# Performance work log

Measured on AMD Instinct MI355X. Metric: run time of the kernel, lower is better.

The kernel has to match this reference:

```python
import jax, jax.numpy as jnp
import numpy as np

N = 50000      # nodes
E = 1600000    # edges (avg degree 32)
DIN, DH, DOUT = 256, 128, 64


def gcn_conv(x, W, b, row, col, w, n):
    """One GCNConv layer (self-loops already appended to row/col/w).
    row = source nodes, col = target nodes; aggregate at targets."""
    xw = x @ W                                        # [n, d_out]
    deg = jax.ops.segment_sum(w, col, num_segments=n)  # in-degree weighted
    dinv = jnp.where(deg > 0, jax.lax.rsqrt(deg), 0.0)
    norm = dinv[row] * w * dinv[col]                  # [E+n]
    msg = norm[:, None] * xw[row]                     # [E+n, d_out] gather
    out = jax.ops.segment_sum(msg, col, num_segments=n)
    return out + b


def setup_inputs() -> dict:
    key = jax.random.key(0)
    k = jax.random.split(key, 6)
    x = jax.random.normal(k[0], (N, DIN), dtype=jnp.float32)
    edge_index = jax.random.randint(k[1], (2, E), 0, N)
    edge_weight = jax.random.uniform(k[2], (E,), dtype=jnp.float32)
    W1 = jax.random.normal(k[3], (DIN, DH), dtype=jnp.float32) * (1.0 / np.sqrt(DIN))
    b1 = jnp.zeros((DH,), dtype=jnp.float32)
    W2 = jax.random.normal(k[4], (DH, DOUT), dtype=jnp.float32) * (1.0 / np.sqrt(DH))
    b2 = jnp.zeros((DOUT,), dtype=jnp.float32)
    return {"x": x, "edge_index": edge_index, "edge_weight": edge_weight,
            "W1": W1, "b1": b1, "W2": W2, "b2": b2}


def reference(x, edge_index, edge_weight, W1, b1, W2, b2):
    n = x.shape[0]
    loops = jnp.arange(n, dtype=edge_index.dtype)
    row = jnp.concatenate([edge_index[0], loops])
    col = jnp.concatenate([edge_index[1], loops])
    w = jnp.concatenate([edge_weight, jnp.ones((n,), dtype=edge_weight.dtype)])
    h = gcn_conv(x, W1, b1, row, col, w, n)
    h = jax.nn.relu(h)
    # dropout(p=0.2) is identity in eval mode
    h = gcn_conv(h, W2, b2, row, col, w, n)
    return jax.nn.log_softmax(h, axis=-1)
```

## Files before the change

### kernel.cpp

```cpp
#include <hip/hip_runtime.h>
#include <hip/hip_bf16.h>
#include <hip/hip_fp16.h>
#include <cstddef>


#define DIN 256
#define DH  128
#define DOUT 64
#define NPB 100
#define NBMAX 512

typedef __bf16 bf16x8 __attribute__((ext_vector_type(8)));
typedef float f32x4 __attribute__((ext_vector_type(4)));

__device__ __forceinline__ float bflo(unsigned u) { return __uint_as_float(u << 16); }
__device__ __forceinline__ float bfhi(unsigned u) { return __uint_as_float(u & 0xffff0000u); }
__device__ __forceinline__ unsigned short f2bf(float f) {
    unsigned u = __float_as_uint(f);
    unsigned r = (u + 0x7fffu + ((u >> 16) & 1u)) >> 16;
    return (unsigned short)r;
}
__device__ __forceinline__ float wdec(unsigned rec) {
    return __half2float(__ushort_as_half((unsigned short)(rec >> 16)));
}

__launch_bounds__(256)
__global__ void kernelA(const int* __restrict__ col, int* __restrict__ bh,
                        int E, int Ec, int NB, int P,
                        const float* __restrict__ W1, const float* __restrict__ W2,
                        unsigned short* __restrict__ wt1, unsigned short* __restrict__ wt2) {
    int blk = blockIdx.x, t = threadIdx.x;
    if (blk < P) {
        __shared__ int hist[NBMAX];
        for (int b = t; b < NB; b += 256) hist[b] = 0;
        __syncthreads();
        int s = blk * Ec, e = min(s + Ec, E);
        for (int i = s + t; i < e; i += 256) atomicAdd(&hist[col[i] / NPB], 1);
        __syncthreads();
        for (int b = t; b < NB; b += 256) bh[blk * NB + b] = hist[b];
    } else {
        int i = (blk - P) * 256 + t;
        if (i < DH * DIN) {
            int nn = i >> 8, k = i & 255;
            wt1[i] = f2bf(W1[k * DH + nn]);
        } else {
            int j = i - DH * DIN;
            if (j < DOUT * DH) {
                int nn = j >> 7, k = j & 127;
                wt2[j] = f2bf(W2[k * DOUT + nn]);
            }
        }
    }
}

__launch_bounds__(512)
__global__ void colscan_kernel(int* __restrict__ bh, int* __restrict__ btotal,
                               int P, int NB) {
    __shared__ int arr[512];
    int b = blockIdx.x, t = threadIdx.x;
    arr[t] = (t < P) ? bh[t * NB + b] : 0;
    __syncthreads();
    for (int off = 1; off < 512; off <<= 1) {
        int v = (t >= off) ? arr[t - off] : 0;
        __syncthreads();
        arr[t] += v;
        __syncthreads();
    }
    int excl = (t == 0) ? 0 : arr[t - 1];
    if (t < P) bh[t * NB + b] = excl;
    if (t == P - 1) btotal[b] = arr[t];
}

__launch_bounds__(256)
__global__ void scatter_kernel(const int* __restrict__ row, const int* __restrict__ col,
                               const float* __restrict__ w, const int* __restrict__ bh,
                               const int* __restrict__ btotal, int* __restrict__ bbase,
                               int* __restrict__ rowptr, int2* __restrict__ part,
                               int E, int Ec, int NB, int n) {
    __shared__ int ps[256];
    __shared__ int bb[NBMAX];
    __shared__ int cur[NBMAX];
    int p = blockIdx.x, t = threadIdx.x;
    int i0 = 2 * t, i1 = 2 * t + 1;
    int x0 = (i0 < NB) ? btotal[i0] : 0;
    int x1 = (i1 < NB) ? btotal[i1] : 0;
    int s = x0 + x1;
    ps[t] = s;
    __syncthreads();
    for (int off = 1; off < 256; off <<= 1) {
        int v = (t >= off) ? ps[t - off] : 0;
        __syncthreads();
        ps[t] += v;
        __syncthreads();
    }
    int excl = ps[t] - s;
    if (i0 < NB) bb[i0] = excl;
    if (i1 < NB) bb[i1] = excl + x0;
    __syncthreads();
    for (int b = t; b < NB; b += 256) cur[b] = bb[b] + bh[p * NB + b];
    if (p == 0) {
        if (i0 < NB) bbase[i0] = bb[i0];
        if (i1 < NB) bbase[i1] = bb[i1];
        if (t == 255) { bbase[NB] = ps[255]; rowptr[n] = E; }
    }
    __syncthreads();
    int s0 = p * Ec, e = min(s0 + Ec, E);
    for (int i = s0 + t; i < e; i += 256) {
        int c = col[i];
        int r = row[i];
        int b = c / NPB;
        int pos = atomicAdd(&cur[b], 1);
        part[pos] = make_int2(r | ((c - b * NPB) << 16), __float_as_int(w[i]));
    }
}

__launch_bounds__(256)
__global__ void bucket_csr_kernel(const int2* __restrict__ part, const int* __restrict__ bbase,
                                  float* __restrict__ dinv, int* __restrict__ rowptr,
                                  unsigned* __restrict__ final_e, int n) {
    __shared__ int   hist[NPB];
    __shared__ float wsum[NPB];
    __shared__ int   nbase[NPB];
    __shared__ int   cur[NPB];
    int b = blockIdx.x, t = threadIdx.x;
    if (t < NPB) { hist[t] = 0; wsum[t] = 0.0f; }
    __syncthreads();
    int s = bbase[b], e = bbase[b + 1];
    for (int i = s + t; i < e; i += 256) {
        int2 rec = part[i];
        int cl = rec.x >> 16;
        atomicAdd(&hist[cl], 1);
        atomicAdd(&wsum[cl], __int_as_float(rec.y));
    }
    __syncthreads();
    if (t == 0) {
        int run = 0;
        for (int k = 0; k < NPB; ++k) { nbase[k] = run; run += hist[k]; }
    }
    __syncthreads();
    if (t < NPB) {
        int node = b * NPB + t;
        if (node < n) {
            dinv[node] = rsqrtf(1.0f + wsum[t]);
            rowptr[node] = s + nbase[t];
        }
        cur[t] = nbase[t];
    }
    __syncthreads();
    for (int i = s + t; i < e; i += 256) {
        int2 rec = part[i];
        int cl = rec.x >> 16;
        int q = s + atomicAdd(&cur[cl], 1);
        unsigned short ws = __half_as_ushort(__float2half_rn(__int_as_float(rec.y)));
        final_e[q] = ((unsigned)rec.x & 0xffffu) | ((unsigned)ws << 16);
    }
}

template <int K, int M, bool ABF16>
__launch_bounds__(256)
__global__ void gemm_mfma_kernel(const void* __restrict__ Av,
                                 const unsigned short* __restrict__ Wt,
                                 const float* __restrict__ scale,
                                 unsigned short* __restrict__ C, int N) {
    constexpr int BK = 64, LD = BK + 8;
    constexpr int WN = M / 4;
    constexpr int NT = WN / 16;
    constexpr int CLD = M + 8;
    constexpr int SM = (64 * LD + M * LD) > (64 * CLD) ? (64 * LD + M * LD) : (64 * CLD);
    __shared__ unsigned short smem[SM];
    __shared__ float sdv[64];
    unsigned short* As = smem;
    unsigned short* Bs = smem + 64 * LD;

    const int tid = threadIdx.x;
    const int row0 = blockIdx.x * 64;
    const int lane = tid & 63;
    const int quad = lane >> 4, r16 = lane & 15;
    const int n0 = (tid >> 6) * WN;

    if (tid < 64) {
        int r = row0 + tid;
        sdv[tid] = (r < N) ? scale[r] : 0.0f;
    }

    f32x4 acc[4][NT];
#pragma unroll
    for (int mt = 0; mt < 4; ++mt)
#pragma unroll
        for (int nt = 0; nt < NT; ++nt)
            acc[mt][nt] = (f32x4){0.f, 0.f, 0.f, 0.f};

    for (int k0 = 0; k0 < K; k0 += BK) {
        if constexpr (ABF16) {
            const unsigned short* A = (const unsigned short*)Av;
#pragma unroll
            for (int j = 0; j < 2; ++j) {
                int idx = tid + j * 256;
                int m = idx >> 3;
                int q = idx & 7;
                int gr = row0 + m;
                uint4 v = make_uint4(0, 0, 0, 0);
                if (gr < N) v = *(const uint4*)&A[(size_t)gr * K + k0 + q * 8];
                *(uint4*)&As[m * LD + q * 8] = v;
            }
        } else {
            const float* A = (const float*)Av;
#pragma unroll
            for (int j = 0; j < 4; ++j) {
                int idx = tid + j * 256;
                int m = idx >> 4;
                int q = idx & 15;
                int gr = row0 + m;
                float4 v = make_float4(0.f, 0.f, 0.f, 0.f);
                if (gr < N) v = *(const float4*)&A[(size_t)gr * K + k0 + q * 4];
                ushort4 s4;
                s4.x = f2bf(v.x); s4.y = f2bf(v.y); s4.z = f2bf(v.z); s4.w = f2bf(v.w);
                *(ushort4*)&As[m * LD + q * 4] = s4;
            }
        }
#pragma unroll
        for (int j = 0; j < M * 8 / 256; ++j) {
            int idx = tid + j * 256;
            int nn = idx >> 3;
            int q = idx & 7;
            uint4 v = *(const uint4*)&Wt[(size_t)nn * K + k0 + q * 8];
            *(uint4*)&Bs[nn * LD + q * 8] = v;
        }
        __syncthreads();
#pragma unroll
        for (int ks = 0; ks < BK / 32; ++ks) {
            bf16x8 af[4], bfr[NT];
#pragma unroll
            for (int nt = 0; nt < NT; ++nt)
                bfr[nt] = *(const bf16x8*)&Bs[(n0 + nt * 16 + r16) * LD + ks * 32 + quad * 8];
#pragma unroll
            for (int mt = 0; mt < 4; ++mt)
                af[mt] = *(const bf16x8*)&As[(mt * 16 + r16) * LD + ks * 32 + quad * 8];
#pragma unroll
            for (int mt = 0; mt < 4; ++mt)
#pragma unroll
                for (int nt = 0; nt < NT; ++nt)
                    acc[mt][nt] = __builtin_amdgcn_mfma_f32_16x16x32_bf16(
                        af[mt], bfr[nt], acc[mt][nt], 0, 0, 0);
        }
        __syncthreads();
    }
    unsigned short* Cs = smem;
#pragma unroll
    for (int mt = 0; mt < 4; ++mt) {
#pragma unroll
        for (int i = 0; i < 4; ++i) {
            int r = mt * 16 + quad * 4 + i;
            float sc = sdv[r];
#pragma unroll
            for (int nt = 0; nt < NT; ++nt)
                Cs[r * CLD + n0 + nt * 16 + r16] = f2bf(acc[mt][nt][i] * sc);
        }
    }
    __syncthreads();
#pragma unroll
    for (int j = 0; j < 64 * M / 8 / 256; ++j) {
        int idx = tid + j * 256;
        int r = idx / (M / 8);
        int q = idx % (M / 8);
        int gr = row0 + r;
        if (gr < N) {
            uint4 v = *(const uint4*)&Cs[r * CLD + q * 8];
            *(uint4*)&C[(size_t)gr * M + q * 8] = v;
        }
    }
}

#define ACC8(v, wgt)                                            \
    a0 += (wgt) * bflo((v).x); a1 += (wgt) * bfhi((v).x);       \
    a2 += (wgt) * bflo((v).y); a3 += (wgt) * bfhi((v).y);       \
    a4 += (wgt) * bflo((v).z); a5 += (wgt) * bfhi((v).z);       \
    a6 += (wgt) * bflo((v).w); a7 += (wgt) * bfhi((v).w);

__launch_bounds__(256, 6)
__global__ void agg1_kernel(const unsigned short* __restrict__ xw,
                            const int* __restrict__ rowptr,
                            const unsigned* __restrict__ edge,
                            const float* __restrict__ dinv,
                            const float* __restrict__ bias,
                            unsigned short* __restrict__ out, int n) {
    int node = blockIdx.x * 4 + (threadIdx.x >> 6);
    if (node >= n) return;
    int lane = threadIdx.x & 63;
    int qw = lane >> 4, sub = lane & 15;
    const char* xb = (const char*)xw;
    const unsigned ssub = (unsigned)sub << 4;
    float di = dinv[node];

    float a0 = 0.f, a1 = 0.f, a2 = 0.f, a3 = 0.f;
    float a4 = 0.f, a5 = 0.f, a6 = 0.f, a7 = 0.f;
    if (qw == 0) {
        uint4 u = *(const uint4*)(xb + (((unsigned)node) << 8) + ssub);
        a0 = bflo(u.x); a1 = bfhi(u.x); a2 = bflo(u.y); a3 = bfhi(u.y);
        a4 = bflo(u.z); a5 = bfhi(u.z); a6 = bflo(u.w); a7 = bfhi(u.w);
    }

    int p = rowptr[node], p1 = rowptr[node + 1];
    int sb = 4 * qw;
    unsigned r0, r1, r2, r3;
    uint4 v0, v1, v2, v3;
    bool have = (p + 16 <= p1);
    if (have) {
        const unsigned* rp = edge + p + sb;
        r0 = __builtin_nontemporal_load(rp);
        r1 = __builtin_nontemporal_load(rp + 1);
        r2 = __builtin_nontemporal_load(rp + 2);
        r3 = __builtin_nontemporal_load(rp + 3);
        v0 = *(const uint4*)(xb + ((r0 & 0xffffu) << 8) + ssub);
        v1 = *(const uint4*)(xb + ((r1 & 0xffffu) << 8) + ssub);
        v2 = *(const uint4*)(xb + ((r2 & 0xffffu) << 8) + ssub);
        v3 = *(const uint4*)(xb + ((r3 & 0xffffu) << 8) + ssub);
    }
#pragma unroll 1
    while (have) {
        p += 16;
        bool havn = (p + 16 <= p1);
        unsigned m0 = 0, m1 = 0, m2 = 0, m3 = 0;
        uint4 u0 = {0,0,0,0}, u1 = {0,0,0,0}, u2 = {0,0,0,0}, u3 = {0,0,0,0};
        if (havn) {
            const unsigned* rp = edge + p + sb;
            m0 = __builtin_nontemporal_load(rp);
            m1 = __builtin_nontemporal_load(rp + 1);
            m2 = __builtin_nontemporal_load(rp + 2);
            m3 = __builtin_nontemporal_load(rp + 3);
            u0 = *(const uint4*)(xb + ((m0 & 0xffffu) << 8) + ssub);
            u1 = *(const uint4*)(xb + ((m1 & 0xffffu) << 8) + ssub);
            u2 = *(const uint4*)(xb + ((m2 & 0xffffu) << 8) + ssub);
            u3 = *(const uint4*)(xb + ((m3 & 0xffffu) << 8) + ssub);
        }
        float w0 = wdec(r0), w1 = wdec(r1), w2 = wdec(r2), w3 = wdec(r3);
        ACC8(v0, w0); ACC8(v1, w1); ACC8(v2, w2); ACC8(v3, w3);
        r0 = m0; r1 = m1; r2 = m2; r3 = m3;
        v0 = u0; v1 = u1; v2 = u2; v3 = u3;
        have = havn;
    }
    int rem = p1 - p;
    if (rem > 0) {
        int last = p1 - 1, b = p + sb;
        unsigned e0 = edge[min(b, last)],     e1 = edge[min(b + 1, last)];
        unsigned e2 = edge[min(b + 2, last)], e3 = edge[min(b + 3, last)];
        float w0 = (b     <= last) ? wdec(e0) : 0.f;
        float w1 = (b + 1 <= last) ? wdec(e1) : 0.f;
        float w2 = (b + 2 <= last) ? wdec(e2) : 0.f;
        float w3 = (b + 3 <= last) ? wdec(e3) : 0.f;
        uint4 t0 = *(const uint4*)(xb + ((e0 & 0xffffu) << 8) + ssub);
        uint4 t1 = *(const uint4*)(xb + ((e1 & 0xffffu) << 8) + ssub);
        uint4 t2 = *(const uint4*)(xb + ((e2 & 0xffffu) << 8) + ssub);
        uint4 t3 = *(const uint4*)(xb + ((e3 & 0xffffu) << 8) + ssub);
        ACC8(t0, w0); ACC8(t1, w1); ACC8(t2, w2); ACC8(t3, w3);
    }
    a0 += __shfl_xor(a0, 16); a0 += __shfl_xor(a0, 32);
    a1 += __shfl_xor(a1, 16); a1 += __shfl_xor(a1, 32);
    a2 += __shfl_xor(a2, 16); a2 += __shfl_xor(a2, 32);
    a3 += __shfl_xor(a3, 16); a3 += __shfl_xor(a3, 32);
    a4 += __shfl_xor(a4, 16); a4 += __shfl_xor(a4, 32);
    a5 += __shfl_xor(a5, 16); a5 += __shfl_xor(a5, 32);
    a6 += __shfl_xor(a6, 16); a6 += __shfl_xor(a6, 32);
    a7 += __shfl_xor(a7, 16); a7 += __shfl_xor(a7, 32);
    if (qw < 2) {
        float4 b = ((const float4*)bias)[2 * sub + qw];
        float o0, o1, o2, o3;
        if (qw == 0) { o0 = a0; o1 = a1; o2 = a2; o3 = a3; }
        else         { o0 = a4; o1 = a5; o2 = a6; o3 = a7; }
        o0 = fmaxf(di * o0 + b.x, 0.f);
        o1 = fmaxf(di * o1 + b.y, 0.f);
        o2 = fmaxf(di * o2 + b.z, 0.f);
        o3 = fmaxf(di * o3 + b.w, 0.f);
        ((ushort4*)out)[(size_t)node * 32 + 2 * sub + qw] =
            make_ushort4(f2bf(o0), f2bf(o1), f2bf(o2), f2bf(o3));
    }
}

__launch_bounds__(256, 6)
__global__ void agg2_kernel(const unsigned short* __restrict__ xw,
                            const int* __restrict__ rowptr,
                            const unsigned* __restrict__ edge,
                            const float* __restrict__ dinv,
                            const float* __restrict__ bias,
                            float* __restrict__ out, int n) {
    int node = blockIdx.x * 4 + (threadIdx.x >> 6);
    if (node >= n) return;
    int lane = threadIdx.x & 63;
    int oct = lane >> 3, sub = lane & 7;
    const char* xb = (const char*)xw;
    const unsigned ssub = (unsigned)sub << 4;
    float di = dinv[node];

    float a0 = 0.f, a1 = 0.f, a2 = 0.f, a3 = 0.f;
    float a4 = 0.f, a5 = 0.f, a6 = 0.f, a7 = 0.f;
    if (oct == 0) {
        uint4 u = *(const uint4*)(xb + (((unsigned)node) << 7) + ssub);
        a0 = bflo(u.x); a1 = bfhi(u.x); a2 = bflo(u.y); a3 = bfhi(u.y);
        a4 = bflo(u.z); a5 = bfhi(u.z); a6 = bflo(u.w); a7 = bfhi(u.w);
    }

    int p = rowptr[node], p1 = rowptr[node + 1];
    int sb = 4 * oct;
    unsigned r0, r1, r2, r3;
    uint4 v0, v1, v2, v3;
    bool have = (p + 32 <= p1);
    if (have) {
        const unsigned* rp = edge + p + sb;
        r0 = __builtin_nontemporal_load(rp);
        r1 = __builtin_nontemporal_load(rp + 1);
        r2 = __builtin_nontemporal_load(rp + 2);
        r3 = __builtin_nontemporal_load(rp + 3);
        v0 = *(const uint4*)(xb + ((r0 & 0xffffu) << 7) + ssub);
        v1 = *(const uint4*)(xb + ((r1 & 0xffffu) << 7) + ssub);
        v2 = *(const uint4*)(xb + ((r2 & 0xffffu) << 7) + ssub);
        v3 = *(const uint4*)(xb + ((r3 & 0xffffu) << 7) + ssub);
    }
#pragma unroll 1
    while (have) {
        p += 32;
        bool havn = (p + 32 <= p1);
        unsigned m0 = 0, m1 = 0, m2 = 0, m3 = 0;
        uint4 u0 = {0,0,0,0}, u1 = {0,0,0,0}, u2 = {0,0,0,0}, u3 = {0,0,0,0};
        if (havn) {
            const unsigned* rp = edge + p + sb;
            m0 = __builtin_nontemporal_load(rp);
            m1 = __builtin_nontemporal_load(rp + 1);
            m2 = __builtin_nontemporal_load(rp + 2);
            m3 = __builtin_nontemporal_load(rp + 3);
            u0 = *(const uint4*)(xb + ((m0 & 0xffffu) << 7) + ssub);
            u1 = *(const uint4*)(xb + ((m1 & 0xffffu) << 7) + ssub);
            u2 = *(const uint4*)(xb + ((m2 & 0xffffu) << 7) + ssub);
            u3 = *(const uint4*)(xb + ((m3 & 0xffffu) << 7) + ssub);
        }
        float w0 = wdec(r0), w1 = wdec(r1), w2 = wdec(r2), w3 = wdec(r3);
        ACC8(v0, w0); ACC8(v1, w1); ACC8(v2, w2); ACC8(v3, w3);
        r0 = m0; r1 = m1; r2 = m2; r3 = m3;
        v0 = u0; v1 = u1; v2 = u2; v3 = u3;
        have = havn;
    }
    int rem = p1 - p;
    if (rem > 0) {
        int last = p1 - 1, b = p + sb;
        unsigned e0 = edge[min(b, last)],     e1 = edge[min(b + 1, last)];
        unsigned e2 = edge[min(b + 2, last)], e3 = edge[min(b + 3, last)];
        float w0 = (b     <= last) ? wdec(e0) : 0.f;
        float w1 = (b + 1 <= last) ? wdec(e1) : 0.f;
        float w2 = (b + 2 <= last) ? wdec(e2) : 0.f;
        float w3 = (b + 3 <= last) ? wdec(e3) : 0.f;
        uint4 t0 = *(const uint4*)(xb + ((e0 & 0xffffu) << 7) + ssub);
        uint4 t1 = *(const uint4*)(xb + ((e1 & 0xffffu) << 7) + ssub);
        uint4 t2 = *(const uint4*)(xb + ((e2 & 0xffffu) << 7) + ssub);
        uint4 t3 = *(const uint4*)(xb + ((e3 & 0xffffu) << 7) + ssub);
        ACC8(t0, w0); ACC8(t1, w1); ACC8(t2, w2); ACC8(t3, w3);
    }
    a0 += __shfl_xor(a0, 8); a0 += __shfl_xor(a0, 16); a0 += __shfl_xor(a0, 32);
    a1 += __shfl_xor(a1, 8); a1 += __shfl_xor(a1, 16); a1 += __shfl_xor(a1, 32);
    a2 += __shfl_xor(a2, 8); a2 += __shfl_xor(a2, 16); a2 += __shfl_xor(a2, 32);
    a3 += __shfl_xor(a3, 8); a3 += __shfl_xor(a3, 16); a3 += __shfl_xor(a3, 32);
    a4 += __shfl_xor(a4, 8); a4 += __shfl_xor(a4, 16); a4 += __shfl_xor(a4, 32);
    a5 += __shfl_xor(a5, 8); a5 += __shfl_xor(a5, 16); a5 += __shfl_xor(a5, 32);
    a6 += __shfl_xor(a6, 8); a6 += __shfl_xor(a6, 16); a6 += __shfl_xor(a6, 32);
    a7 += __shfl_xor(a7, 8); a7 += __shfl_xor(a7, 16); a7 += __shfl_xor(a7, 32);
    const float4* bp = (const float4*)bias;
    float4 bl = bp[2 * sub], bh = bp[2 * sub + 1];
    a0 = di * a0 + bl.x; a1 = di * a1 + bl.y; a2 = di * a2 + bl.z; a3 = di * a3 + bl.w;
    a4 = di * a4 + bh.x; a5 = di * a5 + bh.y; a6 = di * a6 + bh.z; a7 = di * a7 + bh.w;
    float m = fmaxf(fmaxf(fmaxf(a0, a1), fmaxf(a2, a3)),
                    fmaxf(fmaxf(a4, a5), fmaxf(a6, a7)));
    m = fmaxf(m, __shfl_xor(m, 4));
    m = fmaxf(m, __shfl_xor(m, 2));
    m = fmaxf(m, __shfl_xor(m, 1));
    float s = __expf(a0 - m) + __expf(a1 - m) + __expf(a2 - m) + __expf(a3 - m)
            + __expf(a4 - m) + __expf(a5 - m) + __expf(a6 - m) + __expf(a7 - m);
    s += __shfl_xor(s, 4);
    s += __shfl_xor(s, 2);
    s += __shfl_xor(s, 1);
    float lse = m + __logf(s);
    if (oct < 2) {
        f32x4 o;
        if (oct == 0) { o.x = a0 - lse; o.y = a1 - lse; o.z = a2 - lse; o.w = a3 - lse; }
        else          { o.x = a4 - lse; o.y = a5 - lse; o.z = a6 - lse; o.w = a7 - lse; }
        __builtin_nontemporal_store(o, (f32x4*)out + (size_t)node * 16 + 2 * sub + oct);
    }
}

extern "C" void kernel_launch(void* const* d_in, const int* in_sizes, int n_in,
                              void* d_out, int out_size, void* d_ws, size_t ws_size,
                              hipStream_t stream) {
    const float* x  = (const float*)d_in[0];
    const int*   ei = (const int*)d_in[1];
    const float* ew = (const float*)d_in[2];
    const float* W1 = (const float*)d_in[3];
    const float* b1 = (const float*)d_in[4];
    const float* W2 = (const float*)d_in[5];
    const float* b2 = (const float*)d_in[6];
    float* out = (float*)d_out;

    const int n = in_sizes[0] / DIN;
    const int E = in_sizes[2];
    const int* row = ei;
    const int* col = ei + E;

    const int NB = (n + NPB - 1) / NPB;
    const int P  = NB;
    const int Ec = (E + P - 1) / P;

    char* ptr = (char*)d_ws;
    auto alloc = [&](size_t bytes) -> void* {
        void* r = (void*)ptr;
        ptr += (bytes + 255) & ~(size_t)255;
        return r;
    };
    int*   bh     = (int*)  alloc((size_t)P * NB * 4);
    int*   btotal = (int*)  alloc((size_t)NB * 4);
    int*   bbase  = (int*)  alloc((size_t)(NB + 1) * 4);
    int*   rowptr = (int*)  alloc((size_t)(n + 1) * 4);
    float* dinv   = (float*)alloc((size_t)n * 4);
    unsigned* edge = (unsigned*)alloc((size_t)E * 4);
    unsigned short* xw1 = (unsigned short*)alloc((size_t)n * DH * 2);
    unsigned short* wt1 = (unsigned short*)alloc((size_t)DH * DIN * 2);
    unsigned short* wt2 = (unsigned short*)alloc((size_t)DOUT * DH * 2);
    char* tail = (char*)alloc((size_t)n * DH * 4);
    int2*  part = (int2*)tail;
    unsigned short* h1 = (unsigned short*)tail;
    unsigned short* xw2 = xw1;

    const int nb_g = (n + 63) / 64;
    const int nb_a = (n + 3) / 4;
    const int prepb = (DH * DIN + DOUT * DH + 255) / 256;

    kernelA<<<P + prepb, 256, 0, stream>>>(col, bh, E, Ec, NB, P, W1, W2, wt1, wt2);
    colscan_kernel<<<NB, 512, 0, stream>>>(bh, btotal, P, NB);
    scatter_kernel<<<P, 256, 0, stream>>>(row, col, ew, bh, btotal, bbase, rowptr, part, E, Ec, NB, n);
    bucket_csr_kernel<<<NB, 256, 0, stream>>>(part, bbase, dinv, rowptr, edge, n);

    gemm_mfma_kernel<DIN, DH, false><<<nb_g, 256, 0, stream>>>(x, wt1, dinv, xw1, n);
    agg1_kernel<<<nb_a, 256, 0, stream>>>(xw1, rowptr, edge, dinv, b1, h1, n);
    gemm_mfma_kernel<DH, DOUT, true><<<nb_g, 256, 0, stream>>>(h1, wt2, dinv, xw2, n);
    agg2_kernel<<<nb_a, 256, 0, stream>>>(xw2, rowptr, edge, dinv, b2, out, n);
}
```

Before: 268.6 us.

## Fuse CSR build kernels into one cooperative kernel with grid syncs

```diff
diff --git a/kernel.cpp b/kernel.cpp
--- a/kernel.cpp
+++ b/kernel.cpp
@@ -1,7 +1,10 @@
 #include <hip/hip_runtime.h>
+#include <hip/hip_cooperative_groups.h>
 #include <hip/hip_bf16.h>
 #include <hip/hip_fp16.h>
 #include <cstddef>
+
+namespace cg = cooperative_groups;
 
 
 #define DIN 256
@@ -25,19 +28,29 @@
 }
 
 __launch_bounds__(256)
-__global__ void kernelA(const int* __restrict__ col, int* __restrict__ bh,
-                        int E, int Ec, int NB, int P,
-                        const float* __restrict__ W1, const float* __restrict__ W2,
-                        unsigned short* __restrict__ wt1, unsigned short* __restrict__ wt2) {
-    int blk = blockIdx.x, t = threadIdx.x;
+__global__ void build_coop(const int* __restrict__ row, const int* __restrict__ col,
+                           const float* __restrict__ ew,
+                           const float* __restrict__ W1, const float* __restrict__ W2,
+                           unsigned short* __restrict__ wt1, unsigned short* __restrict__ wt2,
+                           int* __restrict__ bh, int* __restrict__ btotal,
+                           int* __restrict__ rowptr, int2* __restrict__ part,
+                           unsigned* __restrict__ edge, float* __restrict__ dinv,
+                           int E, int Ec, int NB, int P, int n) {
+    cg::grid_group grid = cg::this_grid();
+    __shared__ int   sA[NBMAX];
+    __shared__ int   sB[NBMAX];
+    __shared__ int   sC[256];
+    __shared__ float sF[NPB];
+    __shared__ int   s_lo, s_hi;
+    const int blk = blockIdx.x, t = threadIdx.x;
+
     if (blk < P) {
-        __shared__ int hist[NBMAX];
-        for (int b = t; b < NB; b += 256) hist[b] = 0;
+        for (int b = t; b < NB; b += 256) sA[b] = 0;
         __syncthreads();
         int s = blk * Ec, e = min(s + Ec, E);
-        for (int i = s + t; i < e; i += 256) atomicAdd(&hist[col[i] / NPB], 1);
-        __syncthreads();
-        for (int b = t; b < NB; b += 256) bh[blk * NB + b] = hist[b];
+        for (int i = s + t; i < e; i += 256) atomicAdd(&sA[col[i] / NPB], 1);
+        __syncthreads();
+        for (int b = t; b < NB; b += 256) bh[blk * NB + b] = sA[b];
     } else {
         int i = (blk - P) * 256 + t;
         if (i < DH * DIN) {
@@ -51,108 +64,116 @@
             }
         }
     }
-}
-
-__launch_bounds__(512)
-__global__ void colscan_kernel(int* __restrict__ bh, int* __restrict__ btotal,
-                               int P, int NB) {
-    __shared__ int arr[512];
-    int b = blockIdx.x, t = threadIdx.x;
-    arr[t] = (t < P) ? bh[t * NB + b] : 0;
-    __syncthreads();
-    for (int off = 1; off < 512; off <<= 1) {
-        int v = (t >= off) ? arr[t - off] : 0;
-        __syncthreads();
-        arr[t] += v;
-        __syncthreads();
-    }
-    int excl = (t == 0) ? 0 : arr[t - 1];
-    if (t < P) bh[t * NB + b] = excl;
-    if (t == P - 1) btotal[b] = arr[t];
-}
-
-__launch_bounds__(256)
-__global__ void scatter_kernel(const int* __restrict__ row, const int* __restrict__ col,
-                               const float* __restrict__ w, const int* __restrict__ bh,
-                               const int* __restrict__ btotal, int* __restrict__ bbase,
-                               int* __restrict__ rowptr, int2* __restrict__ part,
-                               int E, int Ec, int NB, int n) {
-    __shared__ int ps[256];
-    __shared__ int bb[NBMAX];
-    __shared__ int cur[NBMAX];
-    int p = blockIdx.x, t = threadIdx.x;
-    int i0 = 2 * t, i1 = 2 * t + 1;
-    int x0 = (i0 < NB) ? btotal[i0] : 0;
-    int x1 = (i1 < NB) ? btotal[i1] : 0;
-    int s = x0 + x1;
-    ps[t] = s;
-    __syncthreads();
-    for (int off = 1; off < 256; off <<= 1) {
-        int v = (t >= off) ? ps[t - off] : 0;
-        __syncthreads();
-        ps[t] += v;
-        __syncthreads();
-    }
-    int excl = ps[t] - s;
-    if (i0 < NB) bb[i0] = excl;
-    if (i1 < NB) bb[i1] = excl + x0;
-    __syncthreads();
-    for (int b = t; b < NB; b += 256) cur[b] = bb[b] + bh[p * NB + b];
-    if (p == 0) {
-        if (i0 < NB) bbase[i0] = bb[i0];
-        if (i1 < NB) bbase[i1] = bb[i1];
-        if (t == 255) { bbase[NB] = ps[255]; rowptr[n] = E; }
-    }
-    __syncthreads();
-    int s0 = p * Ec, e = min(s0 + Ec, E);
-    for (int i = s0 + t; i < e; i += 256) {
-        int c = col[i];
-        int r = row[i];
-        int b = c / NPB;
-        int pos = atomicAdd(&cur[b], 1);
-        part[pos] = make_int2(r | ((c - b * NPB) << 16), __float_as_int(w[i]));
-    }
-}
-
-__launch_bounds__(256)
-__global__ void bucket_csr_kernel(const int2* __restrict__ part, const int* __restrict__ bbase,
-                                  float* __restrict__ dinv, int* __restrict__ rowptr,
-                                  unsigned* __restrict__ final_e, int n) {
-    __shared__ int   hist[NPB];
-    __shared__ float wsum[NPB];
-    __shared__ int   nbase[NPB];
-    __shared__ int   cur[NPB];
-    int b = blockIdx.x, t = threadIdx.x;
-    if (t < NPB) { hist[t] = 0; wsum[t] = 0.0f; }
-    __syncthreads();
-    int s = bbase[b], e = bbase[b + 1];
-    for (int i = s + t; i < e; i += 256) {
-        int2 rec = part[i];
-        int cl = rec.x >> 16;
-        atomicAdd(&hist[cl], 1);
-        atomicAdd(&wsum[cl], __int_as_float(rec.y));
-    }
-    __syncthreads();
-    if (t == 0) {
-        int run = 0;
-        for (int k = 0; k < NPB; ++k) { nbase[k] = run; run += hist[k]; }
-    }
-    __syncthreads();
-    if (t < NPB) {
-        int node = b * NPB + t;
-        if (node < n) {
-            dinv[node] = rsqrtf(1.0f + wsum[t]);
-            rowptr[node] = s + nbase[t];
-        }
-        cur[t] = nbase[t];
-    }
-    __syncthreads();
-    for (int i = s + t; i < e; i += 256) {
-        int2 rec = part[i];
-        int cl = rec.x >> 16;
-        int q = s + atomicAdd(&cur[cl], 1);
-        unsigned short ws = __half_as_ushort(__float2half_rn(__int_as_float(rec.y)));
-        final_e[q] = ((unsigned)rec.x & 0xffffu) | ((unsigned)ws << 16);
+    __threadfence();
+    grid.sync();
+
+    if (blk < NB) {
+        int b = blk;
+        int i0 = 2 * t, i1 = 2 * t + 1;
+        int x0 = (i0 < P) ? bh[i0 * NB + b] : 0;
+        int x1 = (i1 < P) ? bh[i1 * NB + b] : 0;
+        int s = x0 + x1;
+        sC[t] = s;
+        __syncthreads();
+        for (int off = 1; off < 256; off <<= 1) {
+            int v = (t >= off) ? sC[t - off] : 0;
+            __syncthreads();
+            sC[t] += v;
+            __syncthreads();
+        }
+        int excl = sC[t] - s;
+        if (i0 < P) bh[i0 * NB + b] = excl;
+        if (i1 < P) bh[i1 * NB + b] = excl + x0;
+        if (t == 255) btotal[b] = sC[255];
+    }
+    __threadfence();
+    grid.sync();
+
+    {
+        int i0 = 2 * t, i1 = 2 * t + 1;
+        int x0 = (i0 < NB) ? btotal[i0] : 0;
+        int x1 = (i1 < NB) ? btotal[i1] : 0;
+        int s = x0 + x1;
+        sC[t] = s;
+        __syncthreads();
+        for (int off = 1; off < 256; off <<= 1) {
+            int v = (t >= off) ? sC[t - off] : 0;
+            __syncthreads();
+            sC[t] += v;
+            __syncthreads();
+        }
+        int excl = sC[t] - s;
+        if (i0 < NB) sA[i0] = excl;
+        if (i1 < NB) sA[i1] = excl + x0;
+        __syncthreads();
+        if (blk < P) {
+            for (int b = t; b < NB; b += 256) sB[b] = sA[b] + bh[blk * NB + b];
+            __syncthreads();
+            int s0 = blk * Ec, e = min(s0 + Ec, E);
+            for (int i = s0 + t; i < e; i += 256) {
+                int c = col[i];
+                int r = row[i];
+                int b = c / NPB;
+                int pos = atomicAdd(&sB[b], 1);
+                part[pos] = make_int2(r | ((c - b * NPB) << 16), __float_as_int(ew[i]));
+            }
+        }
+    }
+    __threadfence();
+    grid.sync();
+
+    if (blk < NB) {
+        int b = blk;
+        int i0 = 2 * t, i1 = 2 * t + 1;
+        int x0 = (i0 < NB) ? btotal[i0] : 0;
+        int x1 = (i1 < NB) ? btotal[i1] : 0;
+        int sum2 = x0 + x1;
+        sC[t] = sum2;
+        __syncthreads();
+        for (int off = 1; off < 256; off <<= 1) {
+            int v = (t >= off) ? sC[t - off] : 0;
+            __syncthreads();
+            sC[t] += v;
+            __syncthreads();
+        }
+        int excl = sC[t] - sum2;
+        if (i0 == b) s_lo = excl;
+        if (i1 == b) s_lo = excl + x0;
+        if (i0 == b + 1) s_hi = excl;
+        if (i1 == b + 1) s_hi = excl + x0;
+        if (b + 1 == NB && t == 255) s_hi = sC[255];
+        if (b == 0 && t == 0) rowptr[n] = E;
+        if (t < NPB) { sA[t] = 0; sF[t] = 0.0f; }
+        __syncthreads();
+        int s = s_lo, e = s_hi;
+        for (int i = s + t; i < e; i += 256) {
+            int2 rec = part[i];
+            int cl = rec.x >> 16;
+            atomicAdd(&sA[cl], 1);
+            atomicAdd(&sF[cl], __int_as_float(rec.y));
+        }
+        __syncthreads();
+        if (t == 0) {
+            int run = 0;
+            for (int k = 0; k < NPB; ++k) { sB[k] = run; run += sA[k]; }
+        }
+        __syncthreads();
+        if (t < NPB) {
+            int node = b * NPB + t;
+            if (node < n) {
+                dinv[node] = rsqrtf(1.0f + sF[t]);
+                rowptr[node] = s + sB[t];
+            }
+            sB[NPB + t] = sB[t];
+        }
+        __syncthreads();
+        for (int i = s + t; i < e; i += 256) {
+            int2 rec = part[i];
+            int cl = rec.x >> 16;
+            int q = s + atomicAdd(&sB[NPB + cl], 1);
+            unsigned short ws = __half_as_ushort(__float2half_rn(__int_as_float(rec.y)));
+            edge[q] = ((unsigned)rec.x & 0xffffu) | ((unsigned)ws << 16);
+        }
     }
 }
 
@@ -513,7 +534,6 @@
     };
     int*   bh     = (int*)  alloc((size_t)P * NB * 4);
     int*   btotal = (int*)  alloc((size_t)NB * 4);
-    int*   bbase  = (int*)  alloc((size_t)(NB + 1) * 4);
     int*   rowptr = (int*)  alloc((size_t)(n + 1) * 4);
     float* dinv   = (float*)alloc((size_t)n * 4);
     unsigned* edge = (unsigned*)alloc((size_t)E * 4);
@@ -529,10 +549,19 @@
     const int nb_a = (n + 3) / 4;
     const int prepb = (DH * DIN + DOUT * DH + 255) / 256;
 
-    kernelA<<<P + prepb, 256, 0, stream>>>(col, bh, E, Ec, NB, P, W1, W2, wt1, wt2);
-    colscan_kernel<<<NB, 512, 0, stream>>>(bh, btotal, P, NB);
-    scatter_kernel<<<P, 256, 0, stream>>>(row, col, ew, bh, btotal, bbase, rowptr, part, E, Ec, NB, n);
-    bucket_csr_kernel<<<NB, 256, 0, stream>>>(part, bbase, dinv, rowptr, edge, n);
+    {
+        int En = E, Ecn = Ec, NBn = NB, Pn = P, nn = n;
+        const int* rowp = row; const int* colp = col; const float* ewp = ew;
+        const float* W1p = W1; const float* W2p = W2;
+        unsigned short* wt1p = wt1; unsigned short* wt2p = wt2;
+        int* bhp = bh; int* btp = btotal; int* rpp = rowptr;
+        int2* partp = part; unsigned* edgep = edge; float* dinvp = dinv;
+        void* args[] = { &rowp, &colp, &ewp, &W1p, &W2p, &wt1p, &wt2p,
+                         &bhp, &btp, &rpp, &partp, &edgep, &dinvp,
+                         &En, &Ecn, &NBn, &Pn, &nn };
+        hipLaunchCooperativeKernel((void*)build_coop, dim3(P + prepb), dim3(256),
+                                   args, 0, stream);
+    }
 
     gemm_mfma_kernel<DIN, DH, false><<<nb_g, 256, 0, stream>>>(x, wt1, dinv, xw1, n);
     agg1_kernel<<<nb_a, 256, 0, stream>>>(xw1, rowptr, edge, dinv, b1, h1, n);
```

Measured after the change: 744.3 us. +177.1%, slower.
